# Optimization experiments

Hardware: AMD Instinct MI355X
Metric: run time of the kernel (lower is better)

## Reference

```python
import jax, jax.numpy as jnp
import numpy as np

N_NODES, D_IN, D_OUT = 1_000_000, 128, 128
M_PATHS, N_INST, PATH_LEN, N_ETYPES = 6, 20_000, 4, 6


def setup_inputs() -> dict:
    key = jax.random.key(0)
    ks = jax.random.split(key, 9)
    scale = 1.0 / np.sqrt(D_IN)
    features = jax.random.normal(ks[0], (N_NODES, D_IN), jnp.float32)
    instances = jax.random.randint(ks[1], (M_PATHS, N_INST, PATH_LEN), 0, N_NODES, dtype=jnp.int64)
    edge_types = jax.random.randint(ks[2], (M_PATHS,), 0, N_ETYPES, dtype=jnp.int64)
    W_enc = jax.random.normal(ks[3], (M_PATHS, D_IN, D_OUT), jnp.float32) * scale
    b_enc = jax.random.normal(ks[4], (M_PATHS, D_OUT), jnp.float32) * scale
    W_att = jax.random.normal(ks[5], (N_ETYPES, 2 * D_OUT), jnp.float32) * scale
    b_att = jax.random.normal(ks[6], (N_ETYPES,), jnp.float32) * scale
    w_mp = jax.random.normal(ks[7], (D_OUT,), jnp.float32) * scale
    b_mp = jax.random.normal(ks[8], (), jnp.float32) * scale
    return {"features": features, "W_enc": W_enc, "b_enc": b_enc, "W_att": W_att,
            "b_att": b_att, "w_mp": w_mp, "b_mp": b_mp,
            "instances": instances, "edge_types": edge_types}


def reference(features, W_enc, b_enc, W_att, b_att, w_mp, b_mp, instances, edge_types):
    # Gather node features for every metapath instance: [M, I, L, D]
    gathered = features[instances]
    # Per-metapath linear encoder: [M, I, L, H]
    encoded = jnp.einsum('mild,mdh->milh', gathered, W_enc) + b_enc[:, None, None, :]
    first = encoded[:, :, 0, :]   # [M, I, H]
    last = encoded[:, :, -1, :]   # [M, I, H]
    cat = jnp.concatenate([first, last], axis=-1)  # [M, I, 2H]
    # Edge-type-specific attention (Linear(2H, 1)) selected per metapath
    Wsel = W_att[edge_types]      # [M, 2H]
    bsel = b_att[edge_types]      # [M]
    scores = jnp.einsum('mik,mk->mi', cat, Wsel) + bsel[:, None]  # [M, I]
    w = jax.nn.softmax(jax.nn.leaky_relu(scores, 0.2), axis=1)    # softmax over instances
    mp_out = jnp.einsum('mi,mih->mh', w, last)                    # [M, H]
    # Metapath-level attention
    mp_scores = mp_out @ w_mp + b_mp                              # [M]
    mw = jax.nn.softmax(jax.nn.leaky_relu(mp_scores, 0.2), axis=0)
    out = jnp.sum(mw[:, None] * mp_out, axis=0)                   # [H]
    return jax.nn.elu(out)
```

## Files before the change

### kernel.cpp

```cpp
#include <hip/hip_runtime.h>
#include <hip/hip_bf16.h>
#include <math.h>

#define NPATH 6
#define NINST 20000
#define PLEN 4
#define DFEAT 128
#define TPB1 256
#define WPB 4
#define GPW 4
#define GPB (WPB * GPW)
#define BPP 128
#define GPP (BPP * GPB)
#define RESCALE_THR 8.0f

__device__ __forceinline__ float dot4(float4 a, float4 b) {
    return a.x * b.x + a.y * b.y + a.z * b.z + a.w * b.w;
}

__global__ __launch_bounds__(TPB1, 4) void k_pass1(
    const float* __restrict__ feat, const int* __restrict__ inst,
    const float* __restrict__ W_enc, const float* __restrict__ b_enc,
    const float* __restrict__ W_att, const float* __restrict__ b_att,
    const int* __restrict__ etype,
    float* __restrict__ pV, float* __restrict__ pM, float* __restrict__ pS)
{
    int m    = blockIdx.x / BPP;
    int bw   = blockIdx.x % BPP;
    int tid  = threadIdx.x;
    int wv   = tid >> 6, lane = tid & 63;
    int grp  = lane >> 4, sub = lane & 15;
    int gid  = wv * GPW + grp;
    int g    = bw * GPB + gid;

    __shared__ float swa[2 * DFEAT];
    __shared__ float su1[DFEAT], su2[DFEAT];
    __shared__ float sbc[DFEAT];
    __shared__ float scv;
    __shared__ float sV[GPB][DFEAT + 4];
    __shared__ float sMx[GPB], sSm[GPB];

    const int4* ib4 = (const int4*)(inst + (size_t)m * NINST * PLEN);
    int i = g;
    int4 j0 = ib4[i];
    int4 j1 = ib4[i + GPP];
    int4 j2 = ib4[i + 2 * GPP];

    const float4* r0 = (const float4*)(feat + (size_t)j0.x * DFEAT);
    const float4* r3 = (const float4*)(feat + (size_t)j0.w * DFEAT);
    float4 A0a = r0[sub], A0b = r0[sub + 16];
    float4 A3a = r3[sub], A3b = r3[sub + 16];
    const float4* q0 = (const float4*)(feat + (size_t)j1.x * DFEAT);
    const float4* q3 = (const float4*)(feat + (size_t)j1.w * DFEAT);
    float4 B0a = q0[sub], B0b = q0[sub + 16];
    float4 B3a = q3[sub], B3b = q3[sub + 16];

    int e = etype[m];
    swa[tid] = W_att[(size_t)e * (2 * DFEAT) + tid];
    __syncthreads();
    if (tid < DFEAT) {
        const float4* Wr = (const float4*)(W_enc + ((size_t)m * DFEAT + tid) * DFEAT);
        float s1 = 0.f, s2 = 0.f;
        #pragma unroll 8
        for (int q = 0; q < DFEAT / 4; ++q) {
            float4 w4 = Wr[q];
            s1 += w4.x * swa[4*q]         + w4.y * swa[4*q+1]
                + w4.z * swa[4*q+2]       + w4.w * swa[4*q+3];
            s2 += w4.x * swa[DFEAT+4*q]   + w4.y * swa[DFEAT+4*q+1]
                + w4.z * swa[DFEAT+4*q+2] + w4.w * swa[DFEAT+4*q+3];
        }
        su1[tid] = s1;
        su2[tid] = s2;
        sbc[tid] = b_enc[m * DFEAT + tid] * (swa[tid] + swa[DFEAT + tid]);
    }
    __syncthreads();
    if (tid < 64) {
        float t = sbc[tid] + sbc[tid + 64];
        #pragma unroll
        for (int o = 32; o; o >>= 1) t += __shfl_xor(t, o);
        if (tid == 0) scv = t + b_att[e];
    }
    __syncthreads();

    float4 U1a = ((const float4*)su1)[sub], U1b = ((const float4*)su1)[sub + 16];
    float4 U2a = ((const float4*)su2)[sub], U2b = ((const float4*)su2)[sub + 16];
    float c = scv;

    float mref = 0.f, tmax = -3e38f, sum = 0.f;
    float4 va = make_float4(0.f, 0.f, 0.f, 0.f);
    float4 vb = make_float4(0.f, 0.f, 0.f, 0.f);

#define COMPUTE(R0a, R0b, R3a, R3b)                                          \
    {                                                                        \
        float p = dot4(R0a, U1a) + dot4(R0b, U1b)                            \
                + dot4(R3a, U2a) + dot4(R3b, U2b);                           \
        p += __shfl_xor(p, 1);                                               \
        p += __shfl_xor(p, 2);                                               \
        p += __shfl_xor(p, 4);                                               \
        p += __shfl_xor(p, 8);                                               \
        float s = p + c;                                                     \
        s = s > 0.f ? s : 0.2f * s;                                          \
        tmax = fmaxf(tmax, s);                                               \
        if (tmax > mref + RESCALE_THR) {                                     \
            float r = __expf(mref - tmax);                                   \
            sum *= r;                                                        \
            va.x *= r; va.y *= r; va.z *= r; va.w *= r;                      \
            vb.x *= r; vb.y *= r; vb.z *= r; vb.w *= r;                      \
            mref = tmax;                                                     \
        }                                                                    \
        float pe = __expf(s - mref);                                         \
        sum += pe;                                                           \
        va.x += pe * R3a.x; va.y += pe * R3a.y;                              \
        va.z += pe * R3a.z; va.w += pe * R3a.w;                              \
        vb.x += pe * R3b.x; vb.y += pe * R3b.y;                              \
        vb.z += pe * R3b.z; vb.w += pe * R3b.w;                              \
    }

    while (i + 2 * GPP < NINST) {
        const float4* p0 = (const float4*)(feat + (size_t)j2.x * DFEAT);
        const float4* p3 = (const float4*)(feat + (size_t)j2.w * DFEAT);
        float4 C0a = p0[sub], C0b = p0[sub + 16];
        float4 C3a = p3[sub], C3b = p3[sub + 16];
        int nj = i + 3 * GPP;
        nj = nj < NINST ? nj : NINST - 1;
        int4 j3 = ib4[nj];

        COMPUTE(A0a, A0b, A3a, A3b);

        A0a = B0a; A0b = B0b; A3a = B3a; A3b = B3b;
        B0a = C0a; B0b = C0b; B3a = C3a; B3b = C3b;
        j2 = j3;
        i += GPP;
    }
    COMPUTE(A0a, A0b, A3a, A3b);
    i += GPP;
    if (i < NINST) COMPUTE(B0a, B0b, B3a, B3b);
#undef COMPUTE

    *(float4*)&sV[gid][sub * 4]      = va;
    *(float4*)&sV[gid][64 + sub * 4] = vb;
    if (sub == 0) { sMx[gid] = mref; sSm[gid] = sum; }
    __syncthreads();

    if (tid < DFEAT) {
        float M = sMx[0];
        #pragma unroll
        for (int k = 1; k < GPB; ++k) M = fmaxf(M, sMx[k]);
        float S = 0.f, V = 0.f;
        #pragma unroll
        for (int k = 0; k < GPB; ++k) {
            float ek = __expf(sMx[k] - M);
            S += ek * sSm[k];
            V += ek * sV[k][tid];
        }
        pV[(size_t)blockIdx.x * DFEAT + tid] = V;
        if (tid == 0) { pM[blockIdx.x] = M; pS[blockIdx.x] = S; }
    }
}

__global__ __launch_bounds__(256) void k_tail(
    const float* __restrict__ pV, const float* __restrict__ pM, const float* __restrict__ pS,
    const float* __restrict__ W_enc, const float* __restrict__ b_enc,
    const float* __restrict__ w_mp, const float* __restrict__ b_mp,
    float* __restrict__ mp_out, float* __restrict__ msv,
    int* __restrict__ cnt, float* __restrict__ out)
{
    int m = blockIdx.x, tid = threadIdx.x;
    int d = tid & 127, slice = tid >> 7;

    __shared__ float tmp[BPP];
    __shared__ float eL[BPP];
    __shared__ float sv[2][DFEAT];
    __shared__ float sVn[DFEAT];
    __shared__ float smp[DFEAT];
    __shared__ float sS, sMx;
    __shared__ int   sOld;

    if (tid < BPP) tmp[tid] = pM[m * BPP + tid];
    __syncthreads();
    for (int off = 64; off; off >>= 1) {
        if (tid < off) tmp[tid] = fmaxf(tmp[tid], tmp[tid + off]);
        __syncthreads();
    }
    if (tid == 0) sMx = tmp[0];
    __syncthreads();
    float M = sMx;

    if (tid < BPP) {
        float ek = __expf(pM[m * BPP + tid] - M);
        eL[tid] = ek;
        tmp[tid] = ek * pS[m * BPP + tid];
    }
    __syncthreads();
    for (int off = 64; off; off >>= 1) {
        if (tid < off) tmp[tid] += tmp[tid + off];
        __syncthreads();
    }
    if (tid == 0) sS = tmp[0];
    __syncthreads();
    float Sinv = 1.f / sS;

    float acc = 0.f;
    for (int k = slice; k < BPP; k += 2)
        acc += eL[k] * pV[((size_t)(m * BPP + k)) * DFEAT + d];
    sv[slice][d] = acc;
    __syncthreads();
    if (tid < DFEAT) sVn[tid] = (sv[0][tid] + sv[1][tid]) * Sinv;
    __syncthreads();

    const float* W = W_enc + (size_t)m * DFEAT * DFEAT;
    float gacc = 0.f;
    for (int dd = slice; dd < DFEAT; dd += 2)
        gacc += sVn[dd] * W[(size_t)dd * DFEAT + d];
    __syncthreads();
    sv[slice][d] = gacc;
    __syncthreads();
    if (tid < DFEAT) {
        float t = sv[0][tid] + sv[1][tid] + b_enc[m * DFEAT + tid];
        mp_out[m * DFEAT + tid] = t;
        smp[tid] = t * w_mp[tid];
    }
    __syncthreads();
    if (tid < 64) {
        float t = smp[tid] + smp[tid + 64];
        #pragma unroll
        for (int o = 32; o; o >>= 1) t += __shfl_xor(t, o);
        if (tid == 0) msv[m] = t + b_mp[0];
    }
    __syncthreads();

    __threadfence();
    if (tid == 0) sOld = atomicAdd(cnt, 1);
    __syncthreads();
    if (sOld != NPATH - 1) return;
    __threadfence();

    if (tid < DFEAT) {
        int h = tid;
        float l[NPATH], mx = -3e38f;
        #pragma unroll
        for (int k = 0; k < NPATH; ++k) {
            float x = msv[k];
            x = x > 0.f ? x : 0.2f * x;
            l[k] = x;
            mx = fmaxf(mx, x);
        }
        float s = 0.f;
        #pragma unroll
        for (int k = 0; k < NPATH; ++k) { l[k] = __expf(l[k] - mx); s += l[k]; }
        float o = 0.f;
        #pragma unroll
        for (int k = 0; k < NPATH; ++k) o += (l[k] / s) * mp_out[k * DFEAT + h];
        out[h] = o > 0.f ? o : __expf(o) - 1.f;
    }
}

extern "C" void kernel_launch(void* const* d_in, const int* in_sizes, int n_in,
                              void* d_out, int out_size, void* d_ws, size_t ws_size,
                              hipStream_t stream) {
    const float* features   = (const float*)d_in[0];
    const float* W_enc      = (const float*)d_in[1];
    const float* b_enc      = (const float*)d_in[2];
    const float* W_att      = (const float*)d_in[3];
    const float* b_att      = (const float*)d_in[4];
    const float* w_mp       = (const float*)d_in[5];
    const float* b_mp       = (const float*)d_in[6];
    const int*   instances  = (const int*)d_in[7];
    const int*   edge_types = (const int*)d_in[8];
    float* out = (float*)d_out;
    float* ws  = (float*)d_ws;

    const int nblk = NPATH * BPP;

    float* pV     = ws;
    float* pM     = pV + (size_t)nblk * DFEAT;
    float* pS     = pM + nblk;
    float* mp_out = pS + nblk;
    float* msv    = mp_out + NPATH * DFEAT;
    int*   cnt    = (int*)(msv + 8);

    hipMemsetAsync(cnt, 0, sizeof(int), stream);

    k_pass1<<<nblk, TPB1, 0, stream>>>(features, instances, W_enc, b_enc,
                                       W_att, b_att, edge_types, pV, pM, pS);

    k_tail<<<NPATH, 256, 0, stream>>>(pV, pM, pS, W_enc, b_enc, w_mp, b_mp,
                                      mp_out, msv, cnt, out);
}
```

Baseline: 72.82 us.

## Merge tail into single block, drop atomic counter and memset

The tail kernel now runs as one 512-thread block that loops over all six metapaths serially, keeping per-metapath outputs and scores in shared memory. This removes the hipMemsetAsync launch, the global atomic counter with its thread fences, and the global round trip for mp_out and msv. In exchange the six metapaths no longer run in parallel across blocks. Each iteration splits its work across 4 thread slices instead of 2 to partly make up for that.

Result: slower. 137.5 us (+88.8%).

```diff
diff --git a/kernel.cpp b/kernel.cpp
--- a/kernel.cpp
+++ b/kernel.cpp
@@ -158,89 +158,86 @@
     }
 }
 
-__global__ __launch_bounds__(256) void k_tail(
+__global__ __launch_bounds__(512) void k_tail(
     const float* __restrict__ pV, const float* __restrict__ pM, const float* __restrict__ pS,
     const float* __restrict__ W_enc, const float* __restrict__ b_enc,
     const float* __restrict__ w_mp, const float* __restrict__ b_mp,
-    float* __restrict__ mp_out, float* __restrict__ msv,
-    int* __restrict__ cnt, float* __restrict__ out)
+    float* __restrict__ out)
 {
-    int m = blockIdx.x, tid = threadIdx.x;
+    int tid = threadIdx.x;
     int d = tid & 127, slice = tid >> 7;
 
     __shared__ float tmp[BPP];
     __shared__ float eL[BPP];
-    __shared__ float sv[2][DFEAT];
+    __shared__ float sv[4][DFEAT];
     __shared__ float sVn[DFEAT];
-    __shared__ float smp[DFEAT];
+    __shared__ float mpAll[NPATH][DFEAT];
+    __shared__ float smsv[NPATH];
     __shared__ float sS, sMx;
-    __shared__ int   sOld;
-
-    if (tid < BPP) tmp[tid] = pM[m * BPP + tid];
-    __syncthreads();
-    for (int off = 64; off; off >>= 1) {
-        if (tid < off) tmp[tid] = fmaxf(tmp[tid], tmp[tid + off]);
-        __syncthreads();
-    }
-    if (tid == 0) sMx = tmp[0];
-    __syncthreads();
-    float M = sMx;
-
-    if (tid < BPP) {
-        float ek = __expf(pM[m * BPP + tid] - M);
-        eL[tid] = ek;
-        tmp[tid] = ek * pS[m * BPP + tid];
-    }
-    __syncthreads();
-    for (int off = 64; off; off >>= 1) {
-        if (tid < off) tmp[tid] += tmp[tid + off];
-        __syncthreads();
-    }
-    if (tid == 0) sS = tmp[0];
-    __syncthreads();
-    float Sinv = 1.f / sS;
-
-    float acc = 0.f;
-    for (int k = slice; k < BPP; k += 2)
-        acc += eL[k] * pV[((size_t)(m * BPP + k)) * DFEAT + d];
-    sv[slice][d] = acc;
-    __syncthreads();
-    if (tid < DFEAT) sVn[tid] = (sv[0][tid] + sv[1][tid]) * Sinv;
-    __syncthreads();
-
-    const float* W = W_enc + (size_t)m * DFEAT * DFEAT;
-    float gacc = 0.f;
-    for (int dd = slice; dd < DFEAT; dd += 2)
-        gacc += sVn[dd] * W[(size_t)dd * DFEAT + d];
-    __syncthreads();
-    sv[slice][d] = gacc;
-    __syncthreads();
+
+    for (int m = 0; m < NPATH; ++m) {
+        if (tid < BPP) tmp[tid] = pM[m * BPP + tid];
+        __syncthreads();
+        for (int off = 64; off; off >>= 1) {
+            if (tid < off) tmp[tid] = fmaxf(tmp[tid], tmp[tid + off]);
+            __syncthreads();
+        }
+        if (tid == 0) sMx = tmp[0];
+        __syncthreads();
+        float M = sMx;
+
+        if (tid < BPP) {
+            float ek = __expf(pM[m * BPP + tid] - M);
+            eL[tid] = ek;
+            tmp[tid] = ek * pS[m * BPP + tid];
+        }
+        __syncthreads();
+        for (int off = 64; off; off >>= 1) {
+            if (tid < off) tmp[tid] += tmp[tid + off];
+            __syncthreads();
+        }
+        if (tid == 0) sS = tmp[0];
+        __syncthreads();
+        float Sinv = 1.f / sS;
+
+        float acc = 0.f;
+        for (int k = slice; k < BPP; k += 4)
+            acc += eL[k] * pV[((size_t)(m * BPP + k)) * DFEAT + d];
+        sv[slice][d] = acc;
+        __syncthreads();
+        if (tid < DFEAT)
+            sVn[tid] = (sv[0][tid] + sv[1][tid] + sv[2][tid] + sv[3][tid]) * Sinv;
+        __syncthreads();
+
+        const float* W = W_enc + (size_t)m * DFEAT * DFEAT;
+        float g = 0.f;
+        for (int dd = slice; dd < DFEAT; dd += 4)
+            g += sVn[dd] * W[(size_t)dd * DFEAT + d];
+        __syncthreads();
+        sv[slice][d] = g;
+        __syncthreads();
+        if (tid < DFEAT) {
+            float t = sv[0][tid] + sv[1][tid] + sv[2][tid] + sv[3][tid]
+                    + b_enc[m * DFEAT + tid];
+            mpAll[m][tid] = t;
+            tmp[tid] = t * w_mp[tid];
+        }
+        __syncthreads();
+
+        if (tid < 64) {
+            float t = tmp[tid] + tmp[tid + 64];
+            #pragma unroll
+            for (int o = 32; o; o >>= 1) t += __shfl_xor(t, o);
+            if (tid == 0) smsv[m] = t + b_mp[0];
+        }
+        __syncthreads();
+    }
+
     if (tid < DFEAT) {
-        float t = sv[0][tid] + sv[1][tid] + b_enc[m * DFEAT + tid];
-        mp_out[m * DFEAT + tid] = t;
-        smp[tid] = t * w_mp[tid];
-    }
-    __syncthreads();
-    if (tid < 64) {
-        float t = smp[tid] + smp[tid + 64];
-        #pragma unroll
-        for (int o = 32; o; o >>= 1) t += __shfl_xor(t, o);
-        if (tid == 0) msv[m] = t + b_mp[0];
-    }
-    __syncthreads();
-
-    __threadfence();
-    if (tid == 0) sOld = atomicAdd(cnt, 1);
-    __syncthreads();
-    if (sOld != NPATH - 1) return;
-    __threadfence();
-
-    if (tid < DFEAT) {
-        int h = tid;
         float l[NPATH], mx = -3e38f;
         #pragma unroll
         for (int k = 0; k < NPATH; ++k) {
-            float x = msv[k];
+            float x = smsv[k];
             x = x > 0.f ? x : 0.2f * x;
             l[k] = x;
             mx = fmaxf(mx, x);
@@ -250,8 +247,8 @@
         for (int k = 0; k < NPATH; ++k) { l[k] = __expf(l[k] - mx); s += l[k]; }
         float o = 0.f;
         #pragma unroll
-        for (int k = 0; k < NPATH; ++k) o += (l[k] / s) * mp_out[k * DFEAT + h];
-        out[h] = o > 0.f ? o : __expf(o) - 1.f;
+        for (int k = 0; k < NPATH; ++k) o += (l[k] / s) * mpAll[k][tid];
+        out[tid] = o > 0.f ? o : __expf(o) - 1.f;
     }
 }
 
@@ -272,18 +269,12 @@
 
     const int nblk = NPATH * BPP;
 
-    float* pV     = ws;
-    float* pM     = pV + (size_t)nblk * DFEAT;
-    float* pS     = pM + nblk;
-    float* mp_out = pS + nblk;
-    float* msv    = mp_out + NPATH * DFEAT;
-    int*   cnt    = (int*)(msv + 8);
-
-    hipMemsetAsync(cnt, 0, sizeof(int), stream);
+    float* pV = ws;
+    float* pM = pV + (size_t)nblk * DFEAT;
+    float* pS = pM + nblk;
 
     k_pass1<<<nblk, TPB1, 0, stream>>>(features, instances, W_enc, b_enc,
                                        W_att, b_att, edge_types, pV, pM, pS);
 
-    k_tail<<<NPATH, 256, 0, stream>>>(pV, pM, pS, W_enc, b_enc, w_mp, b_mp,
-                                      mp_out, msv, cnt, out);
-}
+    k_tail<<<1, 512, 0, stream>>>(pV, pM, pS, W_enc, b_enc, w_mp, b_mp, out);
+}
```
